# Optimization experiments

Hardware: AMD Instinct MI355X
Metric: run time of the kernel (lower is better)

The kernel has to match this reference:

```python
import jax, jax.numpy as jnp
import numpy as np

N_NODES = 50000


def _sage_conv(x, src, dst, Wl, bl, Wr):
    # mean aggregation of neighbor (source) features at destination nodes
    msg = x[src]                                              # [E, d]
    agg = jax.ops.segment_sum(msg, dst, num_segments=N_NODES)  # [N, d]
    cnt = jax.ops.segment_sum(jnp.ones((src.shape[0],), x.dtype), dst,
                              num_segments=N_NODES)            # [N]
    agg = agg / jnp.clip(cnt, 1.0)[:, None]
    # lin_l(aggregated) + lin_r(self), bias only on lin_l (PyG default)
    return agg @ Wl + bl + x @ Wr


def setup_inputs() -> dict:
    key = jax.random.key(0)
    ks = jax.random.split(key, 8)
    d = 128
    E = 800000
    x = jax.random.normal(ks[0], (N_NODES, d), dtype=jnp.float32)
    edge_index = jax.random.randint(ks[1], (2, E), 0, N_NODES, dtype=jnp.int64)
    s1 = 1.0 / np.sqrt(d)
    s2 = 1.0 / np.sqrt(32)
    return {
        "x": x,
        "edge_index": edge_index,
        "W1l": jax.random.normal(ks[2], (d, 32), jnp.float32) * s1,
        "b1": jnp.zeros((32,), jnp.float32),
        "W1r": jax.random.normal(ks[3], (d, 32), jnp.float32) * s1,
        "W2l": jax.random.normal(ks[4], (32, 32), jnp.float32) * s2,
        "b2": jnp.zeros((32,), jnp.float32),
        "W2r": jax.random.normal(ks[5], (32, 32), jnp.float32) * s2,
    }


def reference(x, edge_index, W1l, b1, W1r, W2l, b2, W2r):
    src, dst = edge_index[0], edge_index[1]
    h = jax.nn.relu(_sage_conv(x, src, dst, W1l, b1, W1r))
    return _sage_conv(h, src, dst, W2l, b2, W2r)
```

## Files before the change

kernel.cpp:

```cpp
#include <hip/hip_runtime.h>


#define N_NODES 50000
#define NB 782
#define BKS 64
#define GB 256
#define CAPE 1280
#define TILE 3200

__global__ __launch_bounds__(256) void k_front(
    const float* __restrict__ in, const float* __restrict__ Wl,
    const float* __restrict__ Wr, float* __restrict__ z, int N, int K,
    const int* __restrict__ src, const int* __restrict__ dst,
    int* __restrict__ gcnt, int* __restrict__ ebuf, int E) {
  __shared__ union {
    struct { float xs[64 * 68]; float ws[64 * 64]; } p;
    struct { unsigned pe[TILE]; int hist[NB]; int cur[NB]; } b;
  } sm;
  const int t = threadIdx.x;

  if (blockIdx.x < GB) {
    const int chunk = (E + GB - 1) / GB;
    const int e0 = blockIdx.x * chunk;
    int e1 = e0 + chunk;
    if (e1 > E) e1 = E;
    for (int ts = e0; ts < e1; ts += TILE) {
      int te = ts + TILE;
      if (te > e1) te = e1;
      const int n = te - ts;
      for (int i = t; i < NB; i += 256) sm.b.hist[i] = 0;
      __syncthreads();
      for (int i = t; i < n; i += 256) {
        unsigned s = (unsigned)src[ts + i];
        unsigned d = (unsigned)dst[ts + i];
        sm.b.pe[i] = (s << 16) | d;
        atomicAdd(&sm.b.hist[d >> 6], 1);
      }
      __syncthreads();
      for (int c = t; c < NB; c += 256) {
        int h = sm.b.hist[c];
        sm.b.cur[c] = h ? atomicAdd(&gcnt[c], h) : 0;
      }
      __syncthreads();
      for (int i = t; i < n; i += 256) {
        unsigned pe = sm.b.pe[i];
        int d = (int)(pe & 0xFFFFu);
        int s = (int)(pe >> 16);
        int c = d >> 6;
        int p = atomicAdd(&sm.b.cur[c], 1);
        if (p < CAPE) ebuf[(size_t)c * CAPE + p] = (s << 6) | (d & 63);
      }
      __syncthreads();
    }
    return;
  }

  const int n0 = (blockIdx.x - GB) * 64;
  const int nvalid = (N - n0) < 64 ? (N - n0) : 64;
  const int tx = t & 15, ty = t >> 4;
  const int c0 = tx * 4;
  const int nl = ty * 4;

  float acc[4][4];
#pragma unroll
  for (int i = 0; i < 4; i++)
#pragma unroll
    for (int j = 0; j < 4; j++) acc[i][j] = 0.f;

  for (int kc = 0; kc < K; kc += 64) {
    const int KC = (K - kc) < 64 ? (K - kc) : 64;
    for (int i = t; i < KC * 32; i += 256) {
      int k = i >> 5, c = i & 31;
      sm.p.ws[k * 64 + c] = Wl[(size_t)(kc + k) * 32 + c];
      sm.p.ws[k * 64 + 32 + c] = Wr[(size_t)(kc + k) * 32 + c];
    }
    {
      const int kq = KC >> 2;
      const int sh = (KC == 64) ? 4 : 3;
      const int lim = nvalid * kq;
      for (int i = t; i < lim; i += 256) {
        int n = i >> sh, q = i & (kq - 1);
        float4 v = *(const float4*)(in + (size_t)(n0 + n) * K + kc + q * 4);
        *(float4*)(sm.p.xs + n * 68 + q * 4) = v;
      }
    }
    __syncthreads();

    const float* x0 = sm.p.xs + (nl + 0) * 68;
    const float* x1 = sm.p.xs + (nl + 1) * 68;
    const float* x2 = sm.p.xs + (nl + 2) * 68;
    const float* x3 = sm.p.xs + (nl + 3) * 68;
    for (int k = 0; k < KC; k += 4) {
      float4 xa = *(const float4*)(x0 + k);
      float4 xb = *(const float4*)(x1 + k);
      float4 xc = *(const float4*)(x2 + k);
      float4 xd = *(const float4*)(x3 + k);
#pragma unroll
      for (int kk = 0; kk < 4; kk++) {
        float4 w = *(const float4*)(sm.p.ws + (k + kk) * 64 + c0);
        float va = ((const float*)&xa)[kk];
        float vb = ((const float*)&xb)[kk];
        float vc = ((const float*)&xc)[kk];
        float vd = ((const float*)&xd)[kk];
        acc[0][0] += va * w.x; acc[0][1] += va * w.y;
        acc[0][2] += va * w.z; acc[0][3] += va * w.w;
        acc[1][0] += vb * w.x; acc[1][1] += vb * w.y;
        acc[1][2] += vb * w.z; acc[1][3] += vb * w.w;
        acc[2][0] += vc * w.x; acc[2][1] += vc * w.y;
        acc[2][2] += vc * w.z; acc[2][3] += vc * w.w;
        acc[3][0] += vd * w.x; acc[3][1] += vd * w.y;
        acc[3][2] += vd * w.z; acc[3][3] += vd * w.w;
      }
    }
    __syncthreads();
  }
#pragma unroll
  for (int i = 0; i < 4; i++) {
    int node = n0 + nl + i;
    if (node < N) {
      float4 v = make_float4(acc[i][0], acc[i][1], acc[i][2], acc[i][3]);
      *(float4*)(z + (size_t)node * 64 + c0) = v;
    }
  }
}

__global__ __launch_bounds__(512) void k_fagg1(
    const float* __restrict__ zc, const int* __restrict__ ebuf,
    const int* __restrict__ gcnt, const float* __restrict__ b1,
    const float* __restrict__ W2l, const float* __restrict__ W2r,
    float* __restrict__ z2, int N) {
  __shared__ int lds_e[CAPE];
  __shared__ int lds_s[CAPE];
  __shared__ int deg[BKS];
  __shared__ int cur[BKS];
  __shared__ int off[BKS];
  __shared__ float w2p[32 * 64];
  __shared__ float bsh[32];
  const int t = threadIdx.x;
  const int k = blockIdx.x;
  int ne = gcnt[k];
  if (ne > CAPE) ne = CAPE;
  const size_t base = (size_t)k * CAPE;

  for (int i = t; i < ne; i += 512) lds_e[i] = ebuf[base + i];
  if (t < BKS) deg[t] = 0;
  for (int i = t; i < 2048; i += 512) {
    int jj = i >> 6, c = i & 63;
    w2p[i] = (c < 32) ? W2l[jj * 32 + c] : W2r[jj * 32 + (c - 32)];
  }
  if (t < 32) bsh[t] = b1[t];
  __syncthreads();

  for (int i = t; i < ne; i += 512) atomicAdd(&deg[lds_e[i] & 63], 1);
  __syncthreads();

  if (t < 64) {
    int d = deg[t];
    int x = d;
#pragma unroll
    for (int o = 1; o < 64; o <<= 1) {
      int y = __shfl_up(x, o, 64);
      if (t >= o) x += y;
    }
    off[t] = x - d;
    cur[t] = x - d;
  }
  __syncthreads();

  for (int i = t; i < ne; i += 512) {
    int v = lds_e[i];
    int p = atomicAdd(&cur[v & 63], 1);
    lds_s[p] = v >> 6;
  }
  __syncthreads();

  const int g = t >> 5, j = t & 31;
  const int n0 = k << 6;
#pragma unroll
  for (int i = 0; i < 4; i++) {
    const int nl = g * 4 + i;
    const int node = n0 + nl;
    if (node >= N) break;
    const int a = off[nl];
    const int dg = deg[nl];
    const int b = a + dg;
    float a0 = 0.f, a1 = 0.f, a2 = 0.f, a3 = 0.f;
    int e = a;
    for (; e + 4 <= b; e += 4) {
      int s0 = lds_s[e], s1 = lds_s[e + 1], s2 = lds_s[e + 2], s3 = lds_s[e + 3];
      a0 += zc[(size_t)s0 * 64 + j];
      a1 += zc[(size_t)s1 * 64 + j];
      a2 += zc[(size_t)s2 * 64 + j];
      a3 += zc[(size_t)s3 * 64 + j];
    }
    for (; e < b; ++e) a0 += zc[(size_t)lds_s[e] * 64 + j];
    float sum = (a0 + a1) + (a2 + a3);
    float h = sum / (float)(dg > 1 ? dg : 1) + bsh[j] +
              zc[(size_t)node * 64 + 32 + j];
    h = fmaxf(h, 0.f);
    float p0 = 0.f, p1 = 0.f;
#pragma unroll
    for (int jj = 0; jj < 32; jj++) {
      float hj = __shfl(h, jj, 32);
      p0 += hj * w2p[jj * 64 + j];
      p1 += hj * w2p[jj * 64 + 32 + j];
    }
    z2[(size_t)node * 64 + j] = p0;
    z2[(size_t)node * 64 + 32 + j] = p1;
  }
}

__global__ __launch_bounds__(512) void k_fagg2(
    const float* __restrict__ z2, const int* __restrict__ ebuf,
    const int* __restrict__ gcnt, const float* __restrict__ b2,
    float* __restrict__ out, int N) {
  __shared__ int lds_e[CAPE];
  __shared__ int lds_s[CAPE];
  __shared__ int deg[BKS];
  __shared__ int cur[BKS];
  __shared__ int off[BKS];
  __shared__ float bsh[32];
  const int t = threadIdx.x;
  const int k = blockIdx.x;
  int ne = gcnt[k];
  if (ne > CAPE) ne = CAPE;
  const size_t base = (size_t)k * CAPE;

  for (int i = t; i < ne; i += 512) lds_e[i] = ebuf[base + i];
  if (t < BKS) deg[t] = 0;
  if (t < 32) bsh[t] = b2[t];
  __syncthreads();

  for (int i = t; i < ne; i += 512) atomicAdd(&deg[lds_e[i] & 63], 1);
  __syncthreads();

  if (t < 64) {
    int d = deg[t];
    int x = d;
#pragma unroll
    for (int o = 1; o < 64; o <<= 1) {
      int y = __shfl_up(x, o, 64);
      if (t >= o) x += y;
    }
    off[t] = x - d;
    cur[t] = x - d;
  }
  __syncthreads();

  for (int i = t; i < ne; i += 512) {
    int v = lds_e[i];
    int p = atomicAdd(&cur[v & 63], 1);
    lds_s[p] = v >> 6;
  }
  __syncthreads();

  const int g = t >> 5, j = t & 31;
  const int n0 = k << 6;
#pragma unroll
  for (int i = 0; i < 4; i++) {
    const int nl = g * 4 + i;
    const int node = n0 + nl;
    if (node >= N) break;
    const int a = off[nl];
    const int dg = deg[nl];
    const int b = a + dg;
    float a0 = 0.f, a1 = 0.f, a2 = 0.f, a3 = 0.f;
    int e = a;
    for (; e + 4 <= b; e += 4) {
      int s0 = lds_s[e], s1 = lds_s[e + 1], s2 = lds_s[e + 2], s3 = lds_s[e + 3];
      a0 += z2[(size_t)s0 * 64 + j];
      a1 += z2[(size_t)s1 * 64 + j];
      a2 += z2[(size_t)s2 * 64 + j];
      a3 += z2[(size_t)s3 * 64 + j];
    }
    for (; e < b; ++e) a0 += z2[(size_t)lds_s[e] * 64 + j];
    float sum = (a0 + a1) + (a2 + a3);
    float v = sum / (float)(dg > 1 ? dg : 1) + bsh[j] +
              z2[(size_t)node * 64 + 32 + j];
    out[(size_t)node * 32 + j] = v;
  }
}

extern "C" void kernel_launch(void* const* d_in, const int* in_sizes, int n_in,
                              void* d_out, int out_size, void* d_ws,
                              size_t ws_size, hipStream_t stream) {
  const float* x = (const float*)d_in[0];
  const int* ei = (const int*)d_in[1];
  const float* W1l = (const float*)d_in[2];
  const float* b1 = (const float*)d_in[3];
  const float* W1r = (const float*)d_in[4];
  const float* W2l = (const float*)d_in[5];
  const float* b2 = (const float*)d_in[6];
  const float* W2r = (const float*)d_in[7];
  float* out = (float*)d_out;

  const int N = N_NODES;
  const int E = in_sizes[1] / 2;

  float* zc = (float*)d_ws;
  float* zc2 = zc + (size_t)N * 64;
  int* ebuf = (int*)(zc2 + (size_t)N * 64);
  int* gcnt = ebuf + (size_t)NB * CAPE;

  const int* srcp = ei;
  const int* dstp = ei + E;

  const int nblk_proj = (N + 63) / 64;

  hipMemsetAsync(gcnt, 0, NB * sizeof(int), stream);
  k_front<<<GB + nblk_proj, 256, 0, stream>>>(x, W1l, W1r, zc, N, 128, srcp,
                                              dstp, gcnt, ebuf, E);
  k_fagg1<<<NB, 512, 0, stream>>>(zc, ebuf, gcnt, b1, W2l, W2r, zc2, N);
  k_fagg2<<<NB, 512, 0, stream>>>(zc2, ebuf, gcnt, b2, out, N);
}
```

Before: 171.1 us.

## Gather neighbor rows with float4 loads split across edge lanes in both aggregations

The two aggregation kernels now have each wavefront handle a pair of nodes. Eight lanes split each 32-float source row into float4 loads, and eight edge slots are processed in parallel, followed by a shuffle-xor reduction. In the first aggregation the ReLU'd hidden vector is staged in a shared buffer before the layer-2 projection. The goal is wider memory transactions and more loads in flight than the old one-float-per-lane gather. The cost is the extra reduction shuffles and idle lanes when the two nodes have very different degrees.

```diff
diff --git a/kernel.cpp b/kernel.cpp
--- a/kernel.cpp
+++ b/kernel.cpp
@@ -124,6 +124,30 @@
   }
 }
 
+#define SORT_PHASE(EBUF, NE)                                         \
+  for (int i = t; i < (NE); i += 512) lds_e[i] = (EBUF)[base + i];   \
+  if (t < BKS) deg[t] = 0;                                           \
+  __syncthreads();                                                   \
+  for (int i = t; i < (NE); i += 512) atomicAdd(&deg[lds_e[i] & 63], 1); \
+  __syncthreads();                                                   \
+  if (t < 64) {                                                      \
+    int d = deg[t];                                                  \
+    int x = d;                                                       \
+    _Pragma("unroll") for (int o = 1; o < 64; o <<= 1) {             \
+      int y = __shfl_up(x, o, 64);                                   \
+      if (t >= o) x += y;                                            \
+    }                                                                \
+    off[t] = x - d;                                                  \
+    cur[t] = x - d;                                                  \
+  }                                                                  \
+  __syncthreads();                                                   \
+  for (int i = t; i < (NE); i += 512) {                              \
+    int v = lds_e[i];                                                \
+    int p = atomicAdd(&cur[v & 63], 1);                              \
+    lds_s[p] = v >> 6;                                               \
+  }                                                                  \
+  __syncthreads();
+
 __global__ __launch_bounds__(512) void k_fagg1(
     const float* __restrict__ zc, const int* __restrict__ ebuf,
     const int* __restrict__ gcnt, const float* __restrict__ b1,
@@ -135,69 +159,90 @@
   __shared__ int cur[BKS];
   __shared__ int off[BKS];
   __shared__ float w2p[32 * 64];
-  __shared__ float bsh[32];
+  __shared__ __align__(16) float bsh[32];
+  __shared__ __align__(16) float hbuf[BKS * 36];
   const int t = threadIdx.x;
   const int k = blockIdx.x;
   int ne = gcnt[k];
   if (ne > CAPE) ne = CAPE;
   const size_t base = (size_t)k * CAPE;
 
-  for (int i = t; i < ne; i += 512) lds_e[i] = ebuf[base + i];
-  if (t < BKS) deg[t] = 0;
   for (int i = t; i < 2048; i += 512) {
     int jj = i >> 6, c = i & 63;
     w2p[i] = (c < 32) ? W2l[jj * 32 + c] : W2r[jj * 32 + (c - 32)];
   }
   if (t < 32) bsh[t] = b1[t];
+
+  SORT_PHASE(ebuf, ne)
+
+  const float4* zc4 = (const float4*)zc;
+  const int w = t >> 6, l = t & 63;
+  const int es = l >> 3, fi = l & 7;
+  const int n0 = k << 6;
+  const int w8 = w * 8;
+#pragma unroll
+  for (int p = 0; p < 8; p += 2) {
+    const int nA = w8 + p, nB = w8 + p + 1;
+    const int aA = off[nA], dA = deg[nA];
+    const int aB = off[nB], dB = deg[nB];
+    float4 accA = make_float4(0.f, 0.f, 0.f, 0.f);
+    float4 accB = make_float4(0.f, 0.f, 0.f, 0.f);
+    const int mx = dA > dB ? dA : dB;
+    for (int eb = 0; eb < mx; eb += 8) {
+      const int i = eb + es;
+      if (i < dA) {
+        float4 f = zc4[(size_t)lds_s[aA + i] * 16 + fi];
+        accA.x += f.x; accA.y += f.y; accA.z += f.z; accA.w += f.w;
+      }
+      if (i < dB) {
+        float4 f = zc4[(size_t)lds_s[aB + i] * 16 + fi];
+        accB.x += f.x; accB.y += f.y; accB.z += f.z; accB.w += f.w;
+      }
+    }
+#pragma unroll
+    for (int m = 8; m < 64; m <<= 1) {
+      accA.x += __shfl_xor(accA.x, m, 64);
+      accA.y += __shfl_xor(accA.y, m, 64);
+      accA.z += __shfl_xor(accA.z, m, 64);
+      accA.w += __shfl_xor(accA.w, m, 64);
+      accB.x += __shfl_xor(accB.x, m, 64);
+      accB.y += __shfl_xor(accB.y, m, 64);
+      accB.z += __shfl_xor(accB.z, m, 64);
+      accB.w += __shfl_xor(accB.w, m, 64);
+    }
+    if (es == 0) {
+      const float4 b4 = *(const float4*)(bsh + fi * 4);
+      if (n0 + nA < N) {
+        const float rdA = 1.0f / (float)(dA > 1 ? dA : 1);
+        const float4 sA = *(const float4*)(zc + (size_t)(n0 + nA) * 64 + 32 + fi * 4);
+        float4 h;
+        h.x = fmaxf(accA.x * rdA + b4.x + sA.x, 0.f);
+        h.y = fmaxf(accA.y * rdA + b4.y + sA.y, 0.f);
+        h.z = fmaxf(accA.z * rdA + b4.z + sA.z, 0.f);
+        h.w = fmaxf(accA.w * rdA + b4.w + sA.w, 0.f);
+        *(float4*)(hbuf + nA * 36 + fi * 4) = h;
+      }
+      if (n0 + nB < N) {
+        const float rdB = 1.0f / (float)(dB > 1 ? dB : 1);
+        const float4 sB = *(const float4*)(zc + (size_t)(n0 + nB) * 64 + 32 + fi * 4);
+        float4 h;
+        h.x = fmaxf(accB.x * rdB + b4.x + sB.x, 0.f);
+        h.y = fmaxf(accB.y * rdB + b4.y + sB.y, 0.f);
+        h.z = fmaxf(accB.z * rdB + b4.z + sB.z, 0.f);
+        h.w = fmaxf(accB.w * rdB + b4.w + sB.w, 0.f);
+        *(float4*)(hbuf + nB * 36 + fi * 4) = h;
+      }
+    }
+  }
   __syncthreads();
 
-  for (int i = t; i < ne; i += 512) atomicAdd(&deg[lds_e[i] & 63], 1);
-  __syncthreads();
-
-  if (t < 64) {
-    int d = deg[t];
-    int x = d;
-#pragma unroll
-    for (int o = 1; o < 64; o <<= 1) {
-      int y = __shfl_up(x, o, 64);
-      if (t >= o) x += y;
-    }
-    off[t] = x - d;
-    cur[t] = x - d;
-  }
-  __syncthreads();
-
-  for (int i = t; i < ne; i += 512) {
-    int v = lds_e[i];
-    int p = atomicAdd(&cur[v & 63], 1);
-    lds_s[p] = v >> 6;
-  }
-  __syncthreads();
-
   const int g = t >> 5, j = t & 31;
-  const int n0 = k << 6;
 #pragma unroll
   for (int i = 0; i < 4; i++) {
     const int nl = g * 4 + i;
     const int node = n0 + nl;
     if (node >= N) break;
-    const int a = off[nl];
-    const int dg = deg[nl];
-    const int b = a + dg;
-    float a0 = 0.f, a1 = 0.f, a2 = 0.f, a3 = 0.f;
-    int e = a;
-    for (; e + 4 <= b; e += 4) {
-      int s0 = lds_s[e], s1 = lds_s[e + 1], s2 = lds_s[e + 2], s3 = lds_s[e + 3];
-      a0 += zc[(size_t)s0 * 64 + j];
-      a1 += zc[(size_t)s1 * 64 + j];
-      a2 += zc[(size_t)s2 * 64 + j];
-      a3 += zc[(size_t)s3 * 64 + j];
-    }
-    for (; e < b; ++e) a0 += zc[(size_t)lds_s[e] * 64 + j];
-    float sum = (a0 + a1) + (a2 + a3);
-    float h = sum / (float)(dg > 1 ? dg : 1) + bsh[j] +
-              zc[(size_t)node * 64 + 32 + j];
-    h = fmaxf(h, 0.f);
+    const float h = hbuf[nl * 36 + j];
     float p0 = 0.f, p1 = 0.f;
 #pragma unroll
     for (int jj = 0; jj < 32; jj++) {
@@ -219,65 +264,75 @@
   __shared__ int deg[BKS];
   __shared__ int cur[BKS];
   __shared__ int off[BKS];
-  __shared__ float bsh[32];
+  __shared__ __align__(16) float bsh[32];
   const int t = threadIdx.x;
   const int k = blockIdx.x;
   int ne = gcnt[k];
   if (ne > CAPE) ne = CAPE;
   const size_t base = (size_t)k * CAPE;
 
-  for (int i = t; i < ne; i += 512) lds_e[i] = ebuf[base + i];
-  if (t < BKS) deg[t] = 0;
   if (t < 32) bsh[t] = b2[t];
-  __syncthreads();
-
-  for (int i = t; i < ne; i += 512) atomicAdd(&deg[lds_e[i] & 63], 1);
-  __syncthreads();
-
-  if (t < 64) {
-    int d = deg[t];
-    int x = d;
-#pragma unroll
-    for (int o = 1; o < 64; o <<= 1) {
-      int y = __shfl_up(x, o, 64);
-      if (t >= o) x += y;
-    }
-    off[t] = x - d;
-    cur[t] = x - d;
-  }
-  __syncthreads();
-
-  for (int i = t; i < ne; i += 512) {
-    int v = lds_e[i];
-    int p = atomicAdd(&cur[v & 63], 1);
-    lds_s[p] = v >> 6;
-  }
-  __syncthreads();
-
-  const int g = t >> 5, j = t & 31;
+
+  SORT_PHASE(ebuf, ne)
+
+  const float4* z24 = (const float4*)z2;
+  const int w = t >> 6, l = t & 63;
+  const int es = l >> 3, fi = l & 7;
   const int n0 = k << 6;
-#pragma unroll
-  for (int i = 0; i < 4; i++) {
-    const int nl = g * 4 + i;
-    const int node = n0 + nl;
-    if (node >= N) break;
-    const int a = off[nl];
-    const int dg = deg[nl];
-    const int b = a + dg;
-    float a0 = 0.f, a1 = 0.f, a2 = 0.f, a3 = 0.f;
-    int e = a;
-    for (; e + 4 <= b; e += 4) {
-      int s0 = lds_s[e], s1 = lds_s[e + 1], s2 = lds_s[e + 2], s3 = lds_s[e + 3];
-      a0 += z2[(size_t)s0 * 64 + j];
-      a1 += z2[(size_t)s1 * 64 + j];
-      a2 += z2[(size_t)s2 * 64 + j];
-      a3 += z2[(size_t)s3 * 64 + j];
-    }
-    for (; e < b; ++e) a0 += z2[(size_t)lds_s[e] * 64 + j];
-    float sum = (a0 + a1) + (a2 + a3);
-    float v = sum / (float)(dg > 1 ? dg : 1) + bsh[j] +
-              z2[(size_t)node * 64 + 32 + j];
-    out[(size_t)node * 32 + j] = v;
+  const int w8 = w * 8;
+#pragma unroll
+  for (int p = 0; p < 8; p += 2) {
+    const int nA = w8 + p, nB = w8 + p + 1;
+    const int aA = off[nA], dA = deg[nA];
+    const int aB = off[nB], dB = deg[nB];
+    float4 accA = make_float4(0.f, 0.f, 0.f, 0.f);
+    float4 accB = make_float4(0.f, 0.f, 0.f, 0.f);
+    const int mx = dA > dB ? dA : dB;
+    for (int eb = 0; eb < mx; eb += 8) {
+      const int i = eb + es;
+      if (i < dA) {
+        float4 f = z24[(size_t)lds_s[aA + i] * 16 + fi];
+        accA.x += f.x; accA.y += f.y; accA.z += f.z; accA.w += f.w;
+      }
+      if (i < dB) {
+        float4 f = z24[(size_t)lds_s[aB + i] * 16 + fi];
+        accB.x += f.x; accB.y += f.y; accB.z += f.z; accB.w += f.w;
+      }
+    }
+#pragma unroll
+    for (int m = 8; m < 64; m <<= 1) {
+      accA.x += __shfl_xor(accA.x, m, 64);
+      accA.y += __shfl_xor(accA.y, m, 64);
+      accA.z += __shfl_xor(accA.z, m, 64);
+      accA.w += __shfl_xor(accA.w, m, 64);
+      accB.x += __shfl_xor(accB.x, m, 64);
+      accB.y += __shfl_xor(accB.y, m, 64);
+      accB.z += __shfl_xor(accB.z, m, 64);
+      accB.w += __shfl_xor(accB.w, m, 64);
+    }
+    if (es == 0) {
+      const float4 b4 = *(const float4*)(bsh + fi * 4);
+      if (n0 + nA < N) {
+        const float rdA = 1.0f / (float)(dA > 1 ? dA : 1);
+        const float4 sA = *(const float4*)(z2 + (size_t)(n0 + nA) * 64 + 32 + fi * 4);
+        float4 o;
+        o.x = accA.x * rdA + b4.x + sA.x;
+        o.y = accA.y * rdA + b4.y + sA.y;
+        o.z = accA.z * rdA + b4.z + sA.z;
+        o.w = accA.w * rdA + b4.w + sA.w;
+        *(float4*)(out + (size_t)(n0 + nA) * 32 + fi * 4) = o;
+      }
+      if (n0 + nB < N) {
+        const float rdB = 1.0f / (float)(dB > 1 ? dB : 1);
+        const float4 sB = *(const float4*)(z2 + (size_t)(n0 + nB) * 64 + 32 + fi * 4);
+        float4 o;
+        o.x = accB.x * rdB + b4.x + sB.x;
+        o.y = accB.y * rdB + b4.y + sB.y;
+        o.z = accB.z * rdB + b4.z + sB.z;
+        o.w = accB.w * rdB + b4.w + sB.w;
+        *(float4*)(out + (size_t)(n0 + nB) * 32 + fi * 4) = o;
+      }
+    }
   }
 }
 
```

Result: no change. 169.2 us (-1.1%).

## Split projections into separate arrays, vectorize gathers, reuse sorted adjacency in layer two

Applied to the files above, without the earlier changes.

Splits the projected features into separate left and right arrays so each neighbor row is a contiguous 128-byte float4 gather, with 8 threads per node sharing source indices through shuffles. Layer 1 writes its sorted adjacency and per-node offset/degree back to global memory, so the layer-2 kernel skips the bucket re-sort and becomes a light gather kernel with more, smaller blocks. It also vectorizes the edge and ebuf loads with int4 and pads the global bucket counters to one per 32 ints to reduce atomic contention. In exchange it adds an extra global write of the sorted adjacency and node metadata, and relies on 16-byte alignment of the edge chunks, which the chunk rounding is meant to ensure.

```diff
diff --git a/kernel.cpp b/kernel.cpp
--- a/kernel.cpp
+++ b/kernel.cpp
@@ -10,17 +10,18 @@
 
 __global__ __launch_bounds__(256) void k_front(
     const float* __restrict__ in, const float* __restrict__ Wl,
-    const float* __restrict__ Wr, float* __restrict__ z, int N, int K,
-    const int* __restrict__ src, const int* __restrict__ dst,
-    int* __restrict__ gcnt, int* __restrict__ ebuf, int E) {
-  __shared__ union {
+    const float* __restrict__ Wr, float* __restrict__ zl,
+    float* __restrict__ zr, int N, int K, const int* __restrict__ src,
+    const int* __restrict__ dst, int* __restrict__ gcnt,
+    int* __restrict__ ebuf, int E) {
+  __shared__ __align__(16) union {
     struct { float xs[64 * 68]; float ws[64 * 64]; } p;
     struct { unsigned pe[TILE]; int hist[NB]; int cur[NB]; } b;
   } sm;
   const int t = threadIdx.x;
 
   if (blockIdx.x < GB) {
-    const int chunk = (E + GB - 1) / GB;
+    const int chunk = (((E + GB - 1) / GB) + 3) & ~3;
     const int e0 = blockIdx.x * chunk;
     int e1 = e0 + chunk;
     if (e1 > E) e1 = E;
@@ -28,18 +29,38 @@
       int te = ts + TILE;
       if (te > e1) te = e1;
       const int n = te - ts;
+      if (n <= 0) break;
       for (int i = t; i < NB; i += 256) sm.b.hist[i] = 0;
       __syncthreads();
-      for (int i = t; i < n; i += 256) {
-        unsigned s = (unsigned)src[ts + i];
-        unsigned d = (unsigned)dst[ts + i];
-        sm.b.pe[i] = (s << 16) | d;
-        atomicAdd(&sm.b.hist[d >> 6], 1);
+      {
+        const int n4 = n >> 2;
+        const int4* s4 = (const int4*)(src + ts);
+        const int4* d4 = (const int4*)(dst + ts);
+        for (int i = t; i < n4; i += 256) {
+          int4 sv = s4[i];
+          int4 dv = d4[i];
+          int4 pk;
+          pk.x = (sv.x << 16) | dv.x;
+          pk.y = (sv.y << 16) | dv.y;
+          pk.z = (sv.z << 16) | dv.z;
+          pk.w = (sv.w << 16) | dv.w;
+          *(int4*)(sm.b.pe + 4 * i) = pk;
+          atomicAdd(&sm.b.hist[dv.x >> 6], 1);
+          atomicAdd(&sm.b.hist[dv.y >> 6], 1);
+          atomicAdd(&sm.b.hist[dv.z >> 6], 1);
+          atomicAdd(&sm.b.hist[dv.w >> 6], 1);
+        }
+        for (int i = (n4 << 2) + t; i < n; i += 256) {
+          unsigned s = (unsigned)src[ts + i];
+          unsigned d = (unsigned)dst[ts + i];
+          sm.b.pe[i] = (s << 16) | d;
+          atomicAdd(&sm.b.hist[d >> 6], 1);
+        }
       }
       __syncthreads();
       for (int c = t; c < NB; c += 256) {
         int h = sm.b.hist[c];
-        sm.b.cur[c] = h ? atomicAdd(&gcnt[c], h) : 0;
+        sm.b.cur[c] = h ? atomicAdd(&gcnt[c * 32], h) : 0;
       }
       __syncthreads();
       for (int i = t; i < n; i += 256) {
@@ -119,41 +140,50 @@
     int node = n0 + nl + i;
     if (node < N) {
       float4 v = make_float4(acc[i][0], acc[i][1], acc[i][2], acc[i][3]);
-      *(float4*)(z + (size_t)node * 64 + c0) = v;
+      if (c0 < 32)
+        *(float4*)(zl + (size_t)node * 32 + c0) = v;
+      else
+        *(float4*)(zr + (size_t)node * 32 + (c0 - 32)) = v;
     }
   }
 }
 
 __global__ __launch_bounds__(512) void k_fagg1(
-    const float* __restrict__ zc, const int* __restrict__ ebuf,
-    const int* __restrict__ gcnt, const float* __restrict__ b1,
-    const float* __restrict__ W2l, const float* __restrict__ W2r,
-    float* __restrict__ z2, int N) {
-  __shared__ int lds_e[CAPE];
+    const float* __restrict__ zl, const float* __restrict__ zr,
+    int* __restrict__ ebuf, const int* __restrict__ gcnt,
+    const float* __restrict__ b1, const float* __restrict__ W2l,
+    const float* __restrict__ W2r, float* __restrict__ z2l,
+    float* __restrict__ z2r, int2* __restrict__ nod, int N) {
+  __shared__ __align__(16) int lds_e[CAPE];
   __shared__ int lds_s[CAPE];
   __shared__ int deg[BKS];
   __shared__ int cur[BKS];
   __shared__ int off[BKS];
   __shared__ float w2p[32 * 64];
-  __shared__ float bsh[32];
+  __shared__ __align__(16) float bsh[32];
+  __shared__ __align__(16) float hbuf[BKS * 36];
   const int t = threadIdx.x;
   const int k = blockIdx.x;
-  int ne = gcnt[k];
+  int ne = gcnt[k * 32];
   if (ne > CAPE) ne = CAPE;
   const size_t base = (size_t)k * CAPE;
 
-  for (int i = t; i < ne; i += 512) lds_e[i] = ebuf[base + i];
-  if (t < BKS) deg[t] = 0;
   for (int i = t; i < 2048; i += 512) {
     int jj = i >> 6, c = i & 63;
     w2p[i] = (c < 32) ? W2l[jj * 32 + c] : W2r[jj * 32 + (c - 32)];
   }
   if (t < 32) bsh[t] = b1[t];
-  __syncthreads();
-
+
+  {
+    const int ne4 = ne >> 2;
+    const int4* eb4 = (const int4*)(ebuf + base);
+    for (int i = t; i < ne4; i += 512) *(int4*)(lds_e + 4 * i) = eb4[i];
+    for (int i = (ne4 << 2) + t; i < ne; i += 512) lds_e[i] = ebuf[base + i];
+  }
+  if (t < BKS) deg[t] = 0;
+  __syncthreads();
   for (int i = t; i < ne; i += 512) atomicAdd(&deg[lds_e[i] & 63], 1);
   __syncthreads();
-
   if (t < 64) {
     int d = deg[t];
     int x = d;
@@ -166,7 +196,6 @@
     cur[t] = x - d;
   }
   __syncthreads();
-
   for (int i = t; i < ne; i += 512) {
     int v = lds_e[i];
     int p = atomicAdd(&cur[v & 63], 1);
@@ -174,30 +203,50 @@
   }
   __syncthreads();
 
-  const int g = t >> 5, j = t & 31;
+  for (int i = t; i < ne; i += 512) ebuf[base + i] = lds_s[i];
+  if (t < BKS) {
+    int node = (k << 6) + t;
+    if (node < N) nod[node] = make_int2((int)base + off[t], deg[t]);
+  }
+
+  const int g = t >> 3, fi = t & 7;
+  const int node = (k << 6) + g;
+  const int a = off[g], dg = deg[g];
+  const float4* zl4 = (const float4*)zl;
+  float4 acc = make_float4(0.f, 0.f, 0.f, 0.f);
+  for (int b0 = 0; b0 < dg; b0 += 8) {
+    const int myi = b0 + fi;
+    int sidx = (myi < dg) ? lds_s[a + myi] : 0;
+#pragma unroll
+    for (int q = 0; q < 8; q++) {
+      if (b0 + q < dg) {
+        int s = __shfl(sidx, q, 8);
+        float4 f = zl4[(size_t)s * 8 + fi];
+        acc.x += f.x; acc.y += f.y; acc.z += f.z; acc.w += f.w;
+      }
+    }
+  }
+  if (node < N) {
+    const float rd = 1.0f / (float)(dg > 1 ? dg : 1);
+    const float4 b4 = *(const float4*)(bsh + fi * 4);
+    const float4 sA = *(const float4*)(zr + (size_t)node * 32 + fi * 4);
+    float4 h;
+    h.x = fmaxf(acc.x * rd + b4.x + sA.x, 0.f);
+    h.y = fmaxf(acc.y * rd + b4.y + sA.y, 0.f);
+    h.z = fmaxf(acc.z * rd + b4.z + sA.z, 0.f);
+    h.w = fmaxf(acc.w * rd + b4.w + sA.w, 0.f);
+    *(float4*)(hbuf + g * 36 + fi * 4) = h;
+  }
+  __syncthreads();
+
+  const int gg = t >> 5, j = t & 31;
   const int n0 = k << 6;
 #pragma unroll
   for (int i = 0; i < 4; i++) {
-    const int nl = g * 4 + i;
-    const int node = n0 + nl;
-    if (node >= N) break;
-    const int a = off[nl];
-    const int dg = deg[nl];
-    const int b = a + dg;
-    float a0 = 0.f, a1 = 0.f, a2 = 0.f, a3 = 0.f;
-    int e = a;
-    for (; e + 4 <= b; e += 4) {
-      int s0 = lds_s[e], s1 = lds_s[e + 1], s2 = lds_s[e + 2], s3 = lds_s[e + 3];
-      a0 += zc[(size_t)s0 * 64 + j];
-      a1 += zc[(size_t)s1 * 64 + j];
-      a2 += zc[(size_t)s2 * 64 + j];
-      a3 += zc[(size_t)s3 * 64 + j];
-    }
-    for (; e < b; ++e) a0 += zc[(size_t)lds_s[e] * 64 + j];
-    float sum = (a0 + a1) + (a2 + a3);
-    float h = sum / (float)(dg > 1 ? dg : 1) + bsh[j] +
-              zc[(size_t)node * 64 + 32 + j];
-    h = fmaxf(h, 0.f);
+    const int nl = gg * 4 + i;
+    const int nodei = n0 + nl;
+    if (nodei >= N) break;
+    const float h = hbuf[nl * 36 + j];
     float p0 = 0.f, p1 = 0.f;
 #pragma unroll
     for (int jj = 0; jj < 32; jj++) {
@@ -205,80 +254,46 @@
       p0 += hj * w2p[jj * 64 + j];
       p1 += hj * w2p[jj * 64 + 32 + j];
     }
-    z2[(size_t)node * 64 + j] = p0;
-    z2[(size_t)node * 64 + 32 + j] = p1;
+    z2l[(size_t)nodei * 32 + j] = p0;
+    z2r[(size_t)nodei * 32 + j] = p1;
   }
 }
 
-__global__ __launch_bounds__(512) void k_fagg2(
-    const float* __restrict__ z2, const int* __restrict__ ebuf,
-    const int* __restrict__ gcnt, const float* __restrict__ b2,
-    float* __restrict__ out, int N) {
-  __shared__ int lds_e[CAPE];
-  __shared__ int lds_s[CAPE];
-  __shared__ int deg[BKS];
-  __shared__ int cur[BKS];
-  __shared__ int off[BKS];
-  __shared__ float bsh[32];
+__global__ __launch_bounds__(256) void k_fagg2(
+    const float* __restrict__ z2l, const float* __restrict__ z2r,
+    const int* __restrict__ adj, const int2* __restrict__ nod,
+    const float* __restrict__ b2, float* __restrict__ out, int N) {
+  __shared__ __align__(16) float bsh[32];
   const int t = threadIdx.x;
-  const int k = blockIdx.x;
-  int ne = gcnt[k];
-  if (ne > CAPE) ne = CAPE;
-  const size_t base = (size_t)k * CAPE;
-
-  for (int i = t; i < ne; i += 512) lds_e[i] = ebuf[base + i];
-  if (t < BKS) deg[t] = 0;
   if (t < 32) bsh[t] = b2[t];
   __syncthreads();
-
-  for (int i = t; i < ne; i += 512) atomicAdd(&deg[lds_e[i] & 63], 1);
-  __syncthreads();
-
-  if (t < 64) {
-    int d = deg[t];
-    int x = d;
-#pragma unroll
-    for (int o = 1; o < 64; o <<= 1) {
-      int y = __shfl_up(x, o, 64);
-      if (t >= o) x += y;
-    }
-    off[t] = x - d;
-    cur[t] = x - d;
-  }
-  __syncthreads();
-
-  for (int i = t; i < ne; i += 512) {
-    int v = lds_e[i];
-    int p = atomicAdd(&cur[v & 63], 1);
-    lds_s[p] = v >> 6;
-  }
-  __syncthreads();
-
-  const int g = t >> 5, j = t & 31;
-  const int n0 = k << 6;
-#pragma unroll
-  for (int i = 0; i < 4; i++) {
-    const int nl = g * 4 + i;
-    const int node = n0 + nl;
-    if (node >= N) break;
-    const int a = off[nl];
-    const int dg = deg[nl];
-    const int b = a + dg;
-    float a0 = 0.f, a1 = 0.f, a2 = 0.f, a3 = 0.f;
-    int e = a;
-    for (; e + 4 <= b; e += 4) {
-      int s0 = lds_s[e], s1 = lds_s[e + 1], s2 = lds_s[e + 2], s3 = lds_s[e + 3];
-      a0 += z2[(size_t)s0 * 64 + j];
-      a1 += z2[(size_t)s1 * 64 + j];
-      a2 += z2[(size_t)s2 * 64 + j];
-      a3 += z2[(size_t)s3 * 64 + j];
-    }
-    for (; e < b; ++e) a0 += z2[(size_t)lds_s[e] * 64 + j];
-    float sum = (a0 + a1) + (a2 + a3);
-    float v = sum / (float)(dg > 1 ? dg : 1) + bsh[j] +
-              z2[(size_t)node * 64 + 32 + j];
-    out[(size_t)node * 32 + j] = v;
-  }
+  const int g = t >> 3, fi = t & 7;
+  const int node = blockIdx.x * 32 + g;
+  if (node >= N) return;
+  const int2 nd = nod[node];
+  const float4* z24 = (const float4*)z2l;
+  float4 acc = make_float4(0.f, 0.f, 0.f, 0.f);
+  for (int b0 = 0; b0 < nd.y; b0 += 8) {
+    const int myi = b0 + fi;
+    int sidx = (myi < nd.y) ? adj[nd.x + myi] : 0;
+#pragma unroll
+    for (int q = 0; q < 8; q++) {
+      if (b0 + q < nd.y) {
+        int s = __shfl(sidx, q, 8);
+        float4 f = z24[(size_t)s * 8 + fi];
+        acc.x += f.x; acc.y += f.y; acc.z += f.z; acc.w += f.w;
+      }
+    }
+  }
+  const float rd = 1.0f / (float)(nd.y > 1 ? nd.y : 1);
+  const float4 b4 = *(const float4*)(bsh + fi * 4);
+  const float4 sB = *(const float4*)(z2r + (size_t)node * 32 + fi * 4);
+  float4 o;
+  o.x = acc.x * rd + b4.x + sB.x;
+  o.y = acc.y * rd + b4.y + sB.y;
+  o.z = acc.z * rd + b4.z + sB.z;
+  o.w = acc.w * rd + b4.w + sB.w;
+  *(float4*)(out + (size_t)node * 32 + fi * 4) = o;
 }
 
 extern "C" void kernel_launch(void* const* d_in, const int* in_sizes, int n_in,
@@ -297,19 +312,24 @@
   const int N = N_NODES;
   const int E = in_sizes[1] / 2;
 
-  float* zc = (float*)d_ws;
-  float* zc2 = zc + (size_t)N * 64;
-  int* ebuf = (int*)(zc2 + (size_t)N * 64);
+  float* zl = (float*)d_ws;
+  float* zr = zl + (size_t)N * 32;
+  float* z2l = zr + (size_t)N * 32;
+  float* z2r = z2l + (size_t)N * 32;
+  int* ebuf = (int*)(z2r + (size_t)N * 32);
   int* gcnt = ebuf + (size_t)NB * CAPE;
+  int2* nod = (int2*)(gcnt + (size_t)NB * 32);
 
   const int* srcp = ei;
   const int* dstp = ei + E;
 
   const int nblk_proj = (N + 63) / 64;
-
-  hipMemsetAsync(gcnt, 0, NB * sizeof(int), stream);
-  k_front<<<GB + nblk_proj, 256, 0, stream>>>(x, W1l, W1r, zc, N, 128, srcp,
-                                              dstp, gcnt, ebuf, E);
-  k_fagg1<<<NB, 512, 0, stream>>>(zc, ebuf, gcnt, b1, W2l, W2r, zc2, N);
-  k_fagg2<<<NB, 512, 0, stream>>>(zc2, ebuf, gcnt, b2, out, N);
+  const int nblk_f2 = (N + 31) / 32;
+
+  hipMemsetAsync(gcnt, 0, (size_t)NB * 32 * sizeof(int), stream);
+  k_front<<<GB + nblk_proj, 256, 0, stream>>>(x, W1l, W1r, zl, zr, N, 128,
+                                              srcp, dstp, gcnt, ebuf, E);
+  k_fagg1<<<NB, 512, 0, stream>>>(zl, zr, ebuf, gcnt, b1, W2l, W2r, z2l, z2r,
+                                  nod, N);
+  k_fagg2<<<nblk_f2, 256, 0, stream>>>(z2l, z2r, ebuf, nod, b2, out, N);
 }
```

New measurement: 161.7 us. 5.5% less time.
